# Performance work log

Measured on AMD Instinct MI355X. Metric: run time of the kernel, lower is better.

Reference implementation:

```python
import jax, jax.numpy as jnp
from jax import lax
import numpy as np

B, C, H, W = 16, 3, 512, 512
DICE_W, FOCAL_W, SEP_W = 0.5, 0.5, 0.3
GAMMA, IGNORE, SCALE_IDX, SEP_PW, SMOOTH = 2.0, 255, 2, 1.0, 1e-6


def setup_inputs() -> dict:
    key = jax.random.key(0)
    k1, k2 = jax.random.split(key)
    pred = jax.random.normal(k1, (B, C, H, W), dtype=jnp.float32)
    target = jax.random.randint(k2, (B, H, W), 0, C, dtype=jnp.int32)
    class_weights = jnp.array([0.05, 10.0, 3.0], dtype=jnp.float32)
    return {"pred": pred, "target": target, "class_weights": class_weights}


def _connected_components(mask):
    # mask: [B,H,W] bool -> int32 labels (0 = background), 8-connectivity.
    # Iterative max-label propagation; equivalent component partition to
    # cv2.connectedComponents (label IDs differ but partition is identical,
    # which is all the penalty below depends on).
    m = mask.astype(jnp.int32)
    hw = mask.shape[-2] * mask.shape[-1]
    seeds = jnp.arange(1, hw + 1, dtype=jnp.int32).reshape(1, mask.shape[-2], mask.shape[-1])
    lab0 = m * seeds

    def step(lab):
        nb = lax.reduce_window(lab, jnp.int32(0), lax.max, (1, 3, 3), (1, 1, 1), "SAME")
        return m * nb

    def cond(c):
        lab, prev = c
        return jnp.any(lab != prev)

    def body(c):
        lab, _ = c
        return step(lab), lab

    lab, _ = lax.while_loop(cond, body, (step(lab0), lab0))
    return lab


def _pair_penalty(key_lab, val_lab, both):
    # For each key-label > 0: add 1 if >1 distinct val-labels overlap it.
    # Distinct-count>1 over a set of positive ints  <=>  segment max != segment min.
    n = key_lab.shape[-1] + 1  # labels are raw pixel seeds in [0, H*W]
    BIGI = jnp.int32(2 ** 30)
    vmx_in = jnp.where(both, val_lab, 0)
    vmn_in = jnp.where(both, val_lab, BIGI)

    def per(km, vmx, vmn, b):
        mx = jax.ops.segment_max(vmx, km, num_segments=n)
        mn = jax.ops.segment_min(vmn, km, num_segments=n)
        has = jax.ops.segment_sum(b.astype(jnp.int32), km, num_segments=n) > 0
        hit = has & (mx != mn)
        hit = hit.at[0].set(False)  # exclude background key label 0
        return jnp.sum(hit.astype(jnp.float32))

    return jax.vmap(per)(key_lab, vmx_in, vmn_in, both)


def _separation_loss(pred, target):
    probs = jax.nn.softmax(pred, axis=1)
    pred_bin = probs[:, SCALE_IDX] > 0.5          # [B,H,W]
    tgt_bin = target == SCALE_IDX                 # [B,H,W]
    t_lab = _connected_components(tgt_bin).reshape(pred.shape[0], -1)
    p_lab = _connected_components(pred_bin).reshape(pred.shape[0], -1)
    both = (t_lab > 0) & (p_lab > 0)              # overlap pixels
    pen_t = _pair_penalty(t_lab, p_lab, both)     # target comp split across preds
    pen_p = _pair_penalty(p_lab, t_lab, both)     # pred comp merging targets
    valid = jnp.any(t_lab > 0, axis=1)
    n_valid = jnp.sum(valid.astype(jnp.float32))
    pen = jnp.sum(jnp.where(valid, pen_t + pen_p, 0.0))
    pen = jnp.where(n_valid > 0, pen / jnp.maximum(n_valid * 2.0, 1.0), 0.0)
    nonzero = (jnp.sum(tgt_bin) > 0) & (jnp.sum(pred_bin) > 0)
    return SEP_PW * jnp.where(nonzero, pen, 0.0)


def reference(pred, target, class_weights):
    t = target.astype(jnp.int32)
    tc = jnp.clip(t, 0, C - 1)
    logp = jax.nn.log_softmax(pred, axis=1)                       # [B,C,H,W]
    lp_t = jnp.take_along_axis(logp, tc[:, None], axis=1)[:, 0]    # [B,H,W]
    valid = (t != IGNORE).astype(jnp.float32)
    # weighted cross-entropy with ignore_index (torch semantics: /= sum of weights)
    w = class_weights[tc] * valid
    ce = -jnp.sum(w * lp_t) / jnp.sum(w)
    # dice
    probs = jnp.exp(logp)
    oh = jax.nn.one_hot(t, C, dtype=jnp.float32, axis=1)           # [B,C,H,W]
    inter = jnp.sum(probs * oh, axis=(2, 3))
    union = jnp.sum(probs, axis=(2, 3)) + jnp.sum(oh, axis=(2, 3))
    dice = 1.0 - jnp.mean((2.0 * inter + SMOOTH) / (union + SMOOTH))
    # focal
    pt = jnp.exp(lp_t)
    focal_pix = -class_weights[tc] * (1.0 - pt) ** GAMMA * lp_t * valid
    focal = jnp.sum(focal_pix) / (jnp.sum(valid) + 1e-6)
    # instance separation (non-differentiable; binary threshold + CC)
    sep = _separation_loss(lax.stop_gradient(pred), t)
    return ce + DICE_W * dice + FOCAL_W * focal + SEP_W * sep
```

## Files before the change

kernel.cpp:

```cpp
#include <hip/hip_runtime.h>
#include <stdint.h>


#define NB 16
#define NC 3
#define HH 512
#define WW 512
#define HW (HH * WW)
#define NPIX (NB * HW)
#define LOG2_HW 18
#define IGNORE_IDX 255
#define SCALE_IDX 2
#define SENT (-1)

typedef unsigned long long u64;

struct Accum {
  double ce_num, ce_den, focal_num;
  unsigned long long valid_pix;
  double sum_probs[NB * NC];
  double inter[NB * NC];
  unsigned long long cls_cnt[NB * NC];
  int tcount[NB];
  int pcount[NB];
  int pen[NB];
};

struct Partial {
  double d[9];
  unsigned int u[6];
};

__device__ __forceinline__ double wredd(double v) {
#pragma unroll
  for (int o = 32; o > 0; o >>= 1) v += __shfl_down(v, o, 64);
  return v;
}
__device__ __forceinline__ unsigned int wredu(unsigned int v) {
#pragma unroll
  for (int o = 32; o > 0; o >>= 1) v += __shfl_down(v, o, 64);
  return v;
}

__global__ __launch_bounds__(256) void k_main(
    const float* __restrict__ pred, const int* __restrict__ tgt,
    const float* __restrict__ cw, Partial* __restrict__ part,
    u64* __restrict__ tmask, u64* __restrict__ pmask) {
  const int bid = blockIdx.x;
  const int b = bid >> 6;
  const int chunk = bid & 63;
  const int tid = threadIdx.x;
  const float w0 = cw[0], w1 = cw[1], w2 = cw[2];
  const float* __restrict__ pb = pred + (size_t)b * NC * HW;

  float ce_num = 0.f, ce_den = 0.f, focal = 0.f;
  float sp0 = 0.f, sp1 = 0.f, sp2 = 0.f, it0 = 0.f, it1 = 0.f, it2 = 0.f;
  unsigned int c0 = 0, c1 = 0, c2 = 0, vc = 0, tc_cnt = 0, pc_cnt = 0;

#pragma unroll 1
  for (int k = 0; k < 16; ++k) {
    const int i = (chunk << 12) + (k << 8) + tid;
    const int gp = (b << LOG2_HW) + i;
    const float x0 = pb[i];
    const float x1 = pb[i + HW];
    const float x2 = pb[i + 2 * HW];
    const int t = tgt[gp];

    const float m = fmaxf(fmaxf(x0, x1), x2);
    const float e0 = expf(x0 - m), e1 = expf(x1 - m), e2 = expf(x2 - m);
    const float s = e0 + e1 + e2;
    const float ls = logf(s);
    const float inv = 1.0f / s;
    const float p0 = e0 * inv, p1 = e1 * inv, p2 = e2 * inv;

    sp0 += p0; sp1 += p1; sp2 += p2;

    const int tc = (t < 0) ? 0 : ((t > NC - 1) ? NC - 1 : t);
    const float xt = (tc == 0) ? x0 : ((tc == 1) ? x1 : x2);
    const float lpt = (xt - m) - ls;
    const float pt  = (tc == 0) ? p0 : ((tc == 1) ? p1 : p2);
    const float cwt = (tc == 0) ? w0 : ((tc == 1) ? w1 : w2);
    const float valid = (t != IGNORE_IDX) ? 1.0f : 0.0f;
    const float wv = cwt * valid;

    ce_num += wv * (-lpt);
    ce_den += wv;
    const float om = 1.0f - pt;
    focal += cwt * om * om * (-lpt) * valid;
    vc += (t != IGNORE_IDX) ? 1u : 0u;

    if (t >= 0 && t < NC) {
      if (t == 0)      { it0 += p0; c0++; }
      else if (t == 1) { it1 += p1; c1++; }
      else             { it2 += p2; c2++; }
    }

    const bool tb = (t == SCALE_IDX);
    const float p2soft = e2 / s;
    const bool pbit = (p2soft > 0.5f);
    const u64 mt = __ballot(tb);
    const u64 mp = __ballot(pbit);
    if ((tid & 63) == 0) {
      tmask[gp >> 6] = mt;
      pmask[gp >> 6] = mp;
    }
    tc_cnt += tb ? 1u : 0u;
    pc_cnt += pbit ? 1u : 0u;
  }

  __shared__ double sd[4][9];
  __shared__ unsigned int si[4][6];
  const int wvid = tid >> 6, ln = tid & 63;
  const double r0 = wredd((double)ce_num), r1 = wredd((double)ce_den),
               r2 = wredd((double)focal),
               r3 = wredd((double)sp0), r4 = wredd((double)sp1),
               r5 = wredd((double)sp2),
               r6 = wredd((double)it0), r7 = wredd((double)it1),
               r8 = wredd((double)it2);
  const unsigned int u0 = wredu(c0), u1 = wredu(c1), u2 = wredu(c2),
                     u3 = wredu(vc), u4 = wredu(tc_cnt), u5 = wredu(pc_cnt);
  if (ln == 0) {
    sd[wvid][0] = r0; sd[wvid][1] = r1; sd[wvid][2] = r2;
    sd[wvid][3] = r3; sd[wvid][4] = r4; sd[wvid][5] = r5;
    sd[wvid][6] = r6; sd[wvid][7] = r7; sd[wvid][8] = r8;
    si[wvid][0] = u0; si[wvid][1] = u1; si[wvid][2] = u2;
    si[wvid][3] = u3; si[wvid][4] = u4; si[wvid][5] = u5;
  }
  __syncthreads();
  if (tid == 0) {
    Partial p;
    for (int q = 0; q < 9; ++q) p.d[q] = sd[0][q] + sd[1][q] + sd[2][q] + sd[3][q];
    for (int q = 0; q < 6; ++q) p.u[q] = si[0][q] + si[1][q] + si[2][q] + si[3][q];
    part[bid] = p;
  }
}

__global__ __launch_bounds__(1024) void k_reduce(
    const Partial* __restrict__ part, Accum* __restrict__ acc) {
  const int tid = threadIdx.x;
  const int w = tid >> 6, l = tid & 63;
  const Partial p = part[w * 64 + l];
  double d[9];
  unsigned int u[6];
#pragma unroll
  for (int q = 0; q < 9; ++q) d[q] = wredd(p.d[q]);
#pragma unroll
  for (int q = 0; q < 6; ++q) u[q] = wredu(p.u[q]);

  __shared__ double gsd[16][3];
  __shared__ unsigned int gsu[16];
  if (l == 0) {
    acc->sum_probs[w * NC + 0] = d[3];
    acc->sum_probs[w * NC + 1] = d[4];
    acc->sum_probs[w * NC + 2] = d[5];
    acc->inter[w * NC + 0] = d[6];
    acc->inter[w * NC + 1] = d[7];
    acc->inter[w * NC + 2] = d[8];
    acc->cls_cnt[w * NC + 0] = (unsigned long long)u[0];
    acc->cls_cnt[w * NC + 1] = (unsigned long long)u[1];
    acc->cls_cnt[w * NC + 2] = (unsigned long long)u[2];
    acc->tcount[w] = (int)u[4];
    acc->pcount[w] = (int)u[5];
    gsd[w][0] = d[0]; gsd[w][1] = d[1]; gsd[w][2] = d[2];
    gsu[w] = u[3];
  }
  __syncthreads();
  if (tid == 0) {
    double a0 = 0, a1 = 0, a2 = 0;
    unsigned long long av = 0;
    for (int q = 0; q < 16; ++q) {
      a0 += gsd[q][0]; a1 += gsd[q][1]; a2 += gsd[q][2]; av += gsu[q];
    }
    acc->ce_num = a0; acc->ce_den = a1; acc->focal_num = a2; acc->valid_pix = av;
  }
}

__device__ __forceinline__ int find_lds(volatile int* par, int x) {
  int p = par[x];
  while (p != x) { x = p; p = par[x]; }
  return x;
}
__device__ __forceinline__ void unite_lds(int* par, int a, int b) {
  int la = find_lds(par, a);
  int lb = find_lds(par, b);
  while (la != lb) {
    if (la < lb) { int t = la; la = lb; lb = t; }
    const int old = atomicMin(&par[la], lb);
    if (old == la) break;
    la = old;
  }
}

__global__ __launch_bounds__(256) void k_local(
    const u64* __restrict__ tmask, const u64* __restrict__ pmask,
    int* __restrict__ tlab, int* __restrict__ plab,
    int* __restrict__ tconf, int* __restrict__ pconf) {
  const int idx = blockIdx.x;
  const int img = idx >> 7;
  const int rest = idx & 127;
  const int maskid = rest >> 6;
  const int tile = rest & 63;
  const int ty = tile >> 3, tx = tile & 7;
  const u64* __restrict__ mg = (maskid ? pmask : tmask) + (size_t)img * (HW / 64);
  int* __restrict__ lab  = (maskid ? plab : tlab)   + ((size_t)img << LOG2_HW);
  int* __restrict__ conf = (maskid ? pconf : tconf) + ((size_t)img << LOG2_HW);
  const int tid = threadIdx.x;
  const int lane = tid & 63, wv = tid >> 6;

  __shared__ int par[4096];
  __shared__ u64 mw[64];
  if (tid < 64) mw[tid] = mg[(ty * 64 + tid) * 8 + tx];
  __syncthreads();

#pragma unroll 1
  for (int k = 0; k < 16; ++k) {
    const int y = (k << 2) + wv;
    const u64 w = mw[y];
    int v = -1;
    if ((w >> lane) & 1ull) {
      const u64 sa = w & ~(w << 1);
      const u64 le = sa & (~0ull >> (63 - lane));
      v = (y << 6) + (63 - __clzll(le));
    }
    par[(y << 6) + lane] = v;
  }
  __syncthreads();

#pragma unroll 1
  for (int k = 0; k < 16; ++k) {
    const int y = (k << 2) + wv;
    if (y == 0) continue;
    const u64 w = mw[y];
    if (!((w >> lane) & 1ull)) continue;
    if (lane > 0 && ((w >> (lane - 1)) & 1ull)) continue;
    const u64 z = w >> lane;
    const u64 crun = (z & ~(z + 1)) << lane;
    const u64 win = crun | (crun << 1) | (crun >> 1);
    const u64 a = mw[y - 1];
    u64 aw = a & win;
    const u64 sa = a & ~(a << 1);
    const int me = (y << 6) + lane;
    while (aw) {
      const int p = (int)(__ffsll((long long)aw) - 1);
      const u64 le = sa & (~0ull >> (63 - p));
      const int rs = 63 - __clzll(le);
      unite_lds(par, me, ((y - 1) << 6) + rs);
      const u64 za = a >> p;
      aw &= ~((za & ~(za + 1)) << p);
    }
  }
  __syncthreads();

#pragma unroll 1
  for (int k = 0; k < 16; ++k) {
    const int li = (k << 8) + tid;
    const int y = li >> 6, x = li & 63;
    int out = -1;
    if (par[li] >= 0) {
      int r = par[li], p = par[r];
      while (p != r) { r = p; p = par[r]; }
      out = (ty * 64 + (r >> 6)) * WW + tx * 64 + (r & 63);
    }
    const int gi = (ty * 64 + y) * WW + tx * 64 + x;
    lab[gi] = out;
    conf[gi] = 0;
  }
}

__device__ __forceinline__ int lread(int* p) {
  return __hip_atomic_load(p, __ATOMIC_RELAXED, __HIP_MEMORY_SCOPE_AGENT);
}
__device__ __forceinline__ int findroot(int* L, int x) {
  int p = lread(&L[x]);
  while (p != x) { x = p; p = lread(&L[x]); }
  return x;
}
__device__ __forceinline__ void unite(int* L, int a, int b) {
  int la = findroot(L, a);
  int lb = findroot(L, b);
  while (la != lb) {
    if (la < lb) { int t = la; la = lb; lb = t; }
    const int old = atomicMin(&L[la], lb);
    if (old == la) break;
    la = old;
  }
}

__global__ __launch_bounds__(256) void k_border(int* __restrict__ tlab, int* __restrict__ plab) {
  const int t = blockIdx.x * 256 + threadIdx.x;
  const int pos = t & 511;
  const int rest = t >> 9;
  const int line = rest % 21;
  const int rest2 = rest / 21;
  const int maskid = rest2 & 1;
  const int img = rest2 >> 1;
  int* __restrict__ lab = (maskid ? plab : tlab) + ((size_t)img << LOG2_HW);
  if (line < 7) {
    const int i = (((line + 1) << 6) * WW) + pos;
    if (lab[i] < 0) return;
    if (lab[i - WW] >= 0) unite(lab, i, i - WW);
    if (pos > 0 && lab[i - WW - 1] >= 0) unite(lab, i, i - WW - 1);
    if (pos < WW - 1 && lab[i - WW + 1] >= 0) unite(lab, i, i - WW + 1);
  } else if (line < 14) {
    const int i = pos * WW + ((line - 6) << 6);
    if (lab[i] < 0) return;
    if (lab[i - 1] >= 0) unite(lab, i, i - 1);
    if (pos > 0 && lab[i - WW - 1] >= 0) unite(lab, i, i - WW - 1);
  } else {
    if (pos == 0) return;
    const int i = pos * WW + (((line - 13) << 6) - 1);
    if (lab[i] < 0) return;
    if (lab[i - WW + 1] >= 0) unite(lab, i, i - WW + 1);
  }
}

__device__ __forceinline__ void conf_update(int* __restrict__ conf, int key, int val) {
  const int tag = val + 1;
  const int old = atomicCAS(&conf[key], 0, tag);
  if (old == 0 || old == tag || old == SENT) return;
  atomicExch(&conf[key], SENT);
}

__device__ __forceinline__ int chase_compress(int* __restrict__ L, int i) {
  const int p0 = L[i];
  int r = p0, p = L[r];
  if (p == r) return r;
  do { r = p; p = L[r]; } while (p != r);
  L[p0] = r;
  return r;
}

__global__ __launch_bounds__(256) void k_scatter(
    const u64* __restrict__ tmask, const u64* __restrict__ pmask,
    int* __restrict__ tlab, int* __restrict__ plab,
    int* __restrict__ tconf, int* __restrict__ pconf) {
  const int gt = blockIdx.x * 256 + threadIdx.x;
  const int bb = gt >> LOG2_HW;
  const int i = gt & (HW - 1);
  const size_t base = (size_t)bb << LOG2_HW;
  const int lane = threadIdx.x & 63;
  const u64 tw = tmask[gt >> 6];
  const u64 pw = pmask[gt >> 6];
  if ((tw & pw) == 0) return;
  const bool act = ((tw >> lane) & 1ull) & ((pw >> lane) & 1ull);
  if (!act) return;
  const int rt = chase_compress(tlab + base, i);
  const int rp = chase_compress(plab + base, i);
  conf_update(tconf + base, rt, rp);
  conf_update(pconf + base, rp, rt);
}

__global__ __launch_bounds__(256) void k_count(
    const int4* __restrict__ tconf4, const int4* __restrict__ pconf4,
    int* __restrict__ penpart) {
  const int gt = blockIdx.x * 256 + threadIdx.x;
  const int4 a = tconf4[gt];
  const int4 b = pconf4[gt];
  int add = (a.x == SENT) + (a.y == SENT) + (a.z == SENT) + (a.w == SENT)
          + (b.x == SENT) + (b.y == SENT) + (b.z == SENT) + (b.w == SENT);
  const int tid = threadIdx.x, ln = tid & 63, wv = tid >> 6;
#pragma unroll
  for (int o = 32; o > 0; o >>= 1) add += __shfl_down(add, o, 64);
  __shared__ int s4[4];
  if (ln == 0) s4[wv] = add;
  __syncthreads();
  if (tid == 0) penpart[blockIdx.x] = s4[0] + s4[1] + s4[2] + s4[3];
}

__global__ __launch_bounds__(1024) void k_final(
    const Accum* __restrict__ acc, const int* __restrict__ penpart,
    float* __restrict__ out) {
  const int tid = threadIdx.x, w = tid >> 6, l = tid & 63;
  int s = 0;
#pragma unroll
  for (int k = 0; k < 4; ++k) s += penpart[(w << 8) + (k << 6) + l];
#pragma unroll
  for (int o = 32; o > 0; o >>= 1) s += __shfl_down(s, o, 64);
  __shared__ int pens[16];
  if (l == 0) pens[w] = s;
  __syncthreads();
  if (tid != 0) return;

  const double ce = acc->ce_num / acc->ce_den;
  double dsum = 0.0;
  for (int k = 0; k < NB * NC; ++k) {
    const double un = acc->sum_probs[k] + (double)acc->cls_cnt[k];
    dsum += (2.0 * acc->inter[k] + 1e-6) / (un + 1e-6);
  }
  const double dice = 1.0 - dsum / (double)(NB * NC);
  const double focal = acc->focal_num / ((double)acc->valid_pix + 1e-6);
  long long tt = 0, pp = 0;
  int nv = 0;
  double pensum = 0.0;
  for (int b = 0; b < NB; ++b) {
    tt += acc->tcount[b];
    pp += acc->pcount[b];
    if (acc->tcount[b] > 0) { nv++; pensum += (double)pens[b]; }
  }
  double pen = 0.0;
  if (nv > 0) pen = pensum / fmax((double)nv * 2.0, 1.0);
  const double sep = (tt > 0 && pp > 0) ? 1.0  * pen : 0.0;
  *out = (float)(ce + 0.5 * dice + 0.5 * focal + 0.3 * sep);
}

extern "C" void kernel_launch(void* const* d_in, const int* in_sizes, int n_in,
                              void* d_out, int out_size, void* d_ws, size_t ws_size,
                              hipStream_t stream) {
  (void)in_sizes; (void)n_in; (void)out_size; (void)ws_size;
  const float* pred = (const float*)d_in[0];
  const int* tgt = (const int*)d_in[1];
  const float* cw = (const float*)d_in[2];
  float* out = (float*)d_out;

  char* ws = (char*)d_ws;
  Accum* acc = (Accum*)ws;
  size_t off = 2048;
  Partial* part = (Partial*)(ws + off); off += sizeof(Partial) * NB * 64;
  u64* tmask = (u64*)(ws + off); off += NPIX / 8;
  u64* pmask = (u64*)(ws + off); off += NPIX / 8;
  int* tlab  = (int*)(ws + off); off += (size_t)NPIX * 4;
  int* plab  = (int*)(ws + off); off += (size_t)NPIX * 4;
  int* tconf = (int*)(ws + off); off += (size_t)NPIX * 4;
  int* pconf = (int*)(ws + off); off += (size_t)NPIX * 4;
  int* penpart = (int*)(ws + off); off += (size_t)(NPIX / 1024) * 4;

  hipMemsetAsync(acc, 0, sizeof(Accum), stream);

  k_main<<<NB * 64, 256, 0, stream>>>(pred, tgt, cw, part, tmask, pmask);
  k_reduce<<<1, 1024, 0, stream>>>(part, acc);
  k_local<<<NB * 64 * 2, 256, 0, stream>>>(tmask, pmask, tlab, plab, tconf, pconf);
  k_border<<<(NB * 2 * 21 * 512) / 256, 256, 0, stream>>>(tlab, plab);
  k_scatter<<<NPIX / 256, 256, 0, stream>>>(tmask, pmask, tlab, plab, tconf, pconf);
  k_count<<<NPIX / 1024, 256, 0, stream>>>((const int4*)tconf, (const int4*)pconf, penpart);
  k_final<<<1, 1024, 0, stream>>>(acc, penpart, out);
}
```

Measured before the change: 233.3 us.

## Store tile-local 16-bit labels, sparse root records, fuse count into scatter

Per-pixel labels are now 16-bit tile-local root offsets instead of 32-bit global indices. A parent/conflict int2 record is written only at tile roots, and border unions and scatter lookups work on those root records. Conflict counting moves into the scatter kernel through the atomicExch transition, and the reduce and count kernels plus the memset are removed, with reduction folded into the final kernel. This cuts full-image writes and launches, at the cost of more complex root decoding and uninitialized non-root records that rely on only roots ever being touched.

```diff
diff --git a/kernel.cpp b/kernel.cpp
--- a/kernel.cpp
+++ b/kernel.cpp
@@ -12,19 +12,9 @@
 #define IGNORE_IDX 255
 #define SCALE_IDX 2
 #define SENT (-1)
+#define BG16 0xFFFF
 
 typedef unsigned long long u64;
-
-struct Accum {
-  double ce_num, ce_den, focal_num;
-  unsigned long long valid_pix;
-  double sum_probs[NB * NC];
-  double inter[NB * NC];
-  unsigned long long cls_cnt[NB * NC];
-  int tcount[NB];
-  int pcount[NB];
-  int pen[NB];
-};
 
 struct Partial {
   double d[9];
@@ -135,46 +125,6 @@
   }
 }
 
-__global__ __launch_bounds__(1024) void k_reduce(
-    const Partial* __restrict__ part, Accum* __restrict__ acc) {
-  const int tid = threadIdx.x;
-  const int w = tid >> 6, l = tid & 63;
-  const Partial p = part[w * 64 + l];
-  double d[9];
-  unsigned int u[6];
-#pragma unroll
-  for (int q = 0; q < 9; ++q) d[q] = wredd(p.d[q]);
-#pragma unroll
-  for (int q = 0; q < 6; ++q) u[q] = wredu(p.u[q]);
-
-  __shared__ double gsd[16][3];
-  __shared__ unsigned int gsu[16];
-  if (l == 0) {
-    acc->sum_probs[w * NC + 0] = d[3];
-    acc->sum_probs[w * NC + 1] = d[4];
-    acc->sum_probs[w * NC + 2] = d[5];
-    acc->inter[w * NC + 0] = d[6];
-    acc->inter[w * NC + 1] = d[7];
-    acc->inter[w * NC + 2] = d[8];
-    acc->cls_cnt[w * NC + 0] = (unsigned long long)u[0];
-    acc->cls_cnt[w * NC + 1] = (unsigned long long)u[1];
-    acc->cls_cnt[w * NC + 2] = (unsigned long long)u[2];
-    acc->tcount[w] = (int)u[4];
-    acc->pcount[w] = (int)u[5];
-    gsd[w][0] = d[0]; gsd[w][1] = d[1]; gsd[w][2] = d[2];
-    gsu[w] = u[3];
-  }
-  __syncthreads();
-  if (tid == 0) {
-    double a0 = 0, a1 = 0, a2 = 0;
-    unsigned long long av = 0;
-    for (int q = 0; q < 16; ++q) {
-      a0 += gsd[q][0]; a1 += gsd[q][1]; a2 += gsd[q][2]; av += gsu[q];
-    }
-    acc->ce_num = a0; acc->ce_den = a1; acc->focal_num = a2; acc->valid_pix = av;
-  }
-}
-
 __device__ __forceinline__ int find_lds(volatile int* par, int x) {
   int p = par[x];
   while (p != x) { x = p; p = par[x]; }
@@ -193,8 +143,8 @@
 
 __global__ __launch_bounds__(256) void k_local(
     const u64* __restrict__ tmask, const u64* __restrict__ pmask,
-    int* __restrict__ tlab, int* __restrict__ plab,
-    int* __restrict__ tconf, int* __restrict__ pconf) {
+    ushort* __restrict__ tlab16, ushort* __restrict__ plab16,
+    int2* __restrict__ pc_t, int2* __restrict__ pc_p) {
   const int idx = blockIdx.x;
   const int img = idx >> 7;
   const int rest = idx & 127;
@@ -202,8 +152,8 @@
   const int tile = rest & 63;
   const int ty = tile >> 3, tx = tile & 7;
   const u64* __restrict__ mg = (maskid ? pmask : tmask) + (size_t)img * (HW / 64);
-  int* __restrict__ lab  = (maskid ? plab : tlab)   + ((size_t)img << LOG2_HW);
-  int* __restrict__ conf = (maskid ? pconf : tconf) + ((size_t)img << LOG2_HW);
+  ushort* __restrict__ lab = (maskid ? plab16 : tlab16) + (size_t)img * HW;
+  int2* __restrict__ pc   = (maskid ? pc_p : pc_t) + (size_t)img * HW;
   const int tid = threadIdx.x;
   const int lane = tid & 63, wv = tid >> 6;
 
@@ -252,41 +202,57 @@
   __syncthreads();
 
 #pragma unroll 1
-  for (int k = 0; k < 16; ++k) {
-    const int li = (k << 8) + tid;
-    const int y = li >> 6, x = li & 63;
-    int out = -1;
-    if (par[li] >= 0) {
-      int r = par[li], p = par[r];
-      while (p != r) { r = p; p = par[r]; }
-      out = (ty * 64 + (r >> 6)) * WW + tx * 64 + (r & 63);
-    }
-    const int gi = (ty * 64 + y) * WW + tx * 64 + x;
-    lab[gi] = out;
-    conf[gi] = 0;
-  }
-}
-
-__device__ __forceinline__ int lread(int* p) {
-  return __hip_atomic_load(p, __ATOMIC_RELAXED, __HIP_MEMORY_SCOPE_AGENT);
-}
-__device__ __forceinline__ int findroot(int* L, int x) {
-  int p = lread(&L[x]);
-  while (p != x) { x = p; p = lread(&L[x]); }
+  for (int k = 0; k < 4; ++k) {
+    const int lbase = (k << 10) + (tid << 2);
+    const int gy = (ty << 6) + (lbase >> 6);
+    const int gx = (tx << 6) + (lbase & 63);
+    const int gbase = gy * WW + gx;
+    ushort v[4];
+#pragma unroll
+    for (int j = 0; j < 4; ++j) {
+      const int li = lbase + j;
+      int r = par[li];
+      ushort out = BG16;
+      if (r >= 0) {
+        const bool isroot = (r == li);
+        int p = par[r];
+        while (p != r) { r = p; p = par[r]; }
+        out = (ushort)r;
+        if (isroot) pc[gbase + j] = make_int2(gbase + j, 0);
+      }
+      v[j] = out;
+    }
+    *reinterpret_cast<ushort4*>(&lab[gbase]) =
+        make_ushort4(v[0], v[1], v[2], v[3]);
+  }
+}
+
+__device__ __forceinline__ int pc_par(int2* pc, int x) {
+  return __hip_atomic_load(&pc[x].x, __ATOMIC_RELAXED, __HIP_MEMORY_SCOPE_AGENT);
+}
+__device__ __forceinline__ int findroot_pc(int2* pc, int x) {
+  int p = pc_par(pc, x);
+  while (p != x) { x = p; p = pc_par(pc, x); }
   return x;
 }
-__device__ __forceinline__ void unite(int* L, int a, int b) {
-  int la = findroot(L, a);
-  int lb = findroot(L, b);
+__device__ __forceinline__ void unite_pc(int2* pc, int a, int b) {
+  int la = findroot_pc(pc, a);
+  int lb = findroot_pc(pc, b);
   while (la != lb) {
     if (la < lb) { int t = la; la = lb; lb = t; }
-    const int old = atomicMin(&L[la], lb);
+    const int old = atomicMin(&pc[la].x, lb);
     if (old == la) break;
     la = old;
   }
 }
 
-__global__ __launch_bounds__(256) void k_border(int* __restrict__ tlab, int* __restrict__ plab) {
+__device__ __forceinline__ int decode_root(int ty, int tx, int l) {
+  return ((ty << 6) + (l >> 6)) * WW + (tx << 6) + (l & 63);
+}
+
+__global__ __launch_bounds__(256) void k_border(
+    const ushort* __restrict__ tlab16, const ushort* __restrict__ plab16,
+    int2* __restrict__ pc_t, int2* __restrict__ pc_p) {
   const int t = blockIdx.x * 256 + threadIdx.x;
   const int pos = t & 511;
   const int rest = t >> 9;
@@ -294,108 +260,160 @@
   const int rest2 = rest / 21;
   const int maskid = rest2 & 1;
   const int img = rest2 >> 1;
-  int* __restrict__ lab = (maskid ? plab : tlab) + ((size_t)img << LOG2_HW);
+  const ushort* __restrict__ lab = (maskid ? plab16 : tlab16) + (size_t)img * HW;
+  int2* __restrict__ pc = (maskid ? pc_p : pc_t) + (size_t)img * HW;
+
   if (line < 7) {
-    const int i = (((line + 1) << 6) * WW) + pos;
-    if (lab[i] < 0) return;
-    if (lab[i - WW] >= 0) unite(lab, i, i - WW);
-    if (pos > 0 && lab[i - WW - 1] >= 0) unite(lab, i, i - WW - 1);
-    if (pos < WW - 1 && lab[i - WW + 1] >= 0) unite(lab, i, i - WW + 1);
+    const int y = (line + 1) << 6;
+    const int i = y * WW + pos;
+    const ushort li = lab[i];
+    if (li == BG16) return;
+    const int ty = line + 1, tx = pos >> 6;
+    const int gi = decode_root(ty, tx, li);
+    const ushort ln_ = lab[i - WW];
+    if (ln_ != BG16) unite_pc(pc, gi, decode_root(line, tx, ln_));
+    if (pos > 0) {
+      const ushort lw = lab[i - WW - 1];
+      if (lw != BG16) unite_pc(pc, gi, decode_root(line, (pos - 1) >> 6, lw));
+    }
+    if (pos < WW - 1) {
+      const ushort le = lab[i - WW + 1];
+      if (le != BG16) unite_pc(pc, gi, decode_root(line, (pos + 1) >> 6, le));
+    }
   } else if (line < 14) {
-    const int i = pos * WW + ((line - 6) << 6);
-    if (lab[i] < 0) return;
-    if (lab[i - 1] >= 0) unite(lab, i, i - 1);
-    if (pos > 0 && lab[i - WW - 1] >= 0) unite(lab, i, i - WW - 1);
+    const int x = (line - 6) << 6;
+    const int i = pos * WW + x;
+    const ushort li = lab[i];
+    if (li == BG16) return;
+    const int ty = pos >> 6, tx = line - 6;
+    const int gi = decode_root(ty, tx, li);
+    const ushort lw = lab[i - 1];
+    if (lw != BG16) unite_pc(pc, gi, decode_root(ty, tx - 1, lw));
+    if (pos > 0) {
+      const ushort ld = lab[i - WW - 1];
+      if (ld != BG16) unite_pc(pc, gi, decode_root((pos - 1) >> 6, tx - 1, ld));
+    }
   } else {
     if (pos == 0) return;
-    const int i = pos * WW + (((line - 13) << 6) - 1);
-    if (lab[i] < 0) return;
-    if (lab[i - WW + 1] >= 0) unite(lab, i, i - WW + 1);
-  }
-}
-
-__device__ __forceinline__ void conf_update(int* __restrict__ conf, int key, int val) {
+    const int x = ((line - 13) << 6) - 1;
+    const int i = pos * WW + x;
+    const ushort li = lab[i];
+    if (li == BG16) return;
+    const int ty = pos >> 6, tx = x >> 6;
+    const int gi = decode_root(ty, tx, li);
+    const ushort le = lab[i - WW + 1];
+    if (le != BG16) unite_pc(pc, gi, decode_root((pos - 1) >> 6, tx + 1, le));
+  }
+}
+
+__device__ __forceinline__ int chase_pc(int2* __restrict__ pc, int g) {
+  int r = pc[g].x;
+  if (r == g) return r;
+  int p = pc[r].x;
+  while (p != r) { r = p; p = pc[r].x; }
+  pc[g].x = r;
+  return r;
+}
+
+__device__ __forceinline__ int conf_update(int2* __restrict__ pc, int key, int val) {
   const int tag = val + 1;
-  const int old = atomicCAS(&conf[key], 0, tag);
-  if (old == 0 || old == tag || old == SENT) return;
-  atomicExch(&conf[key], SENT);
-}
-
-__device__ __forceinline__ int chase_compress(int* __restrict__ L, int i) {
-  const int p0 = L[i];
-  int r = p0, p = L[r];
-  if (p == r) return r;
-  do { r = p; p = L[r]; } while (p != r);
-  L[p0] = r;
-  return r;
+  const int old = atomicCAS(&pc[key].y, 0, tag);
+  if (old == 0 || old == tag || old == SENT) return 0;
+  const int prev = atomicExch(&pc[key].y, SENT);
+  return (prev != SENT) ? 1 : 0;
 }
 
 __global__ __launch_bounds__(256) void k_scatter(
-    const u64* __restrict__ tmask, const u64* __restrict__ pmask,
-    int* __restrict__ tlab, int* __restrict__ plab,
-    int* __restrict__ tconf, int* __restrict__ pconf) {
-  const int gt = blockIdx.x * 256 + threadIdx.x;
-  const int bb = gt >> LOG2_HW;
-  const int i = gt & (HW - 1);
-  const size_t base = (size_t)bb << LOG2_HW;
-  const int lane = threadIdx.x & 63;
-  const u64 tw = tmask[gt >> 6];
-  const u64 pw = pmask[gt >> 6];
-  if ((tw & pw) == 0) return;
-  const bool act = ((tw >> lane) & 1ull) & ((pw >> lane) & 1ull);
-  if (!act) return;
-  const int rt = chase_compress(tlab + base, i);
-  const int rp = chase_compress(plab + base, i);
-  conf_update(tconf + base, rt, rp);
-  conf_update(pconf + base, rp, rt);
-}
-
-__global__ __launch_bounds__(256) void k_count(
-    const int4* __restrict__ tconf4, const int4* __restrict__ pconf4,
+    const ushort* __restrict__ tlab16, const ushort* __restrict__ plab16,
+    int2* __restrict__ pc_t, int2* __restrict__ pc_p,
     int* __restrict__ penpart) {
-  const int gt = blockIdx.x * 256 + threadIdx.x;
-  const int4 a = tconf4[gt];
-  const int4 b = pconf4[gt];
-  int add = (a.x == SENT) + (a.y == SENT) + (a.z == SENT) + (a.w == SENT)
-          + (b.x == SENT) + (b.y == SENT) + (b.z == SENT) + (b.w == SENT);
+  const int gt4 = blockIdx.x * 256 + threadIdx.x;
+  const int img = gt4 >> (LOG2_HW - 2);
+  const int i0 = (gt4 & ((HW >> 2) - 1)) << 2;
+  const size_t ibase = (size_t)img * HW;
+  const ushort4 t4 = *reinterpret_cast<const ushort4*>(&tlab16[ibase + i0]);
+  const ushort4 p4 = *reinterpret_cast<const ushort4*>(&plab16[ibase + i0]);
+  int2* __restrict__ pct = pc_t + ibase;
+  int2* __restrict__ pcp = pc_p + ibase;
+  const ushort tl[4] = {t4.x, t4.y, t4.z, t4.w};
+  const ushort pl[4] = {p4.x, p4.y, p4.z, p4.w};
+
+  int cnt = 0;
+  const int y = i0 >> 9, ty = y >> 6, txb = (i0 & 511) >> 6;
+#pragma unroll
+  for (int j = 0; j < 4; ++j) {
+    if (tl[j] != BG16 && pl[j] != BG16) {
+      const int gt_root = decode_root(ty, txb, tl[j]);
+      const int gp_root = decode_root(ty, txb, pl[j]);
+      const int rt = chase_pc(pct, gt_root);
+      const int rp = chase_pc(pcp, gp_root);
+      cnt += conf_update(pct, rt, rp);
+      cnt += conf_update(pcp, rp, rt);
+    }
+  }
+
   const int tid = threadIdx.x, ln = tid & 63, wv = tid >> 6;
 #pragma unroll
-  for (int o = 32; o > 0; o >>= 1) add += __shfl_down(add, o, 64);
+  for (int o = 32; o > 0; o >>= 1) cnt += __shfl_down(cnt, o, 64);
   __shared__ int s4[4];
-  if (ln == 0) s4[wv] = add;
+  if (ln == 0) s4[wv] = cnt;
   __syncthreads();
   if (tid == 0) penpart[blockIdx.x] = s4[0] + s4[1] + s4[2] + s4[3];
 }
 
 __global__ __launch_bounds__(1024) void k_final(
-    const Accum* __restrict__ acc, const int* __restrict__ penpart,
+    const Partial* __restrict__ part, const int* __restrict__ penpart,
     float* __restrict__ out) {
   const int tid = threadIdx.x, w = tid >> 6, l = tid & 63;
+  const Partial p = part[w * 64 + l];
+  double d[9];
+  unsigned int u[6];
+#pragma unroll
+  for (int q = 0; q < 9; ++q) d[q] = wredd(p.d[q]);
+#pragma unroll
+  for (int q = 0; q < 6; ++q) u[q] = wredu(p.u[q]);
+
   int s = 0;
 #pragma unroll
   for (int k = 0; k < 4; ++k) s += penpart[(w << 8) + (k << 6) + l];
 #pragma unroll
   for (int o = 32; o > 0; o >>= 1) s += __shfl_down(s, o, 64);
+
+  __shared__ double imgd[16][9];
+  __shared__ unsigned int imgu[16][6];
   __shared__ int pens[16];
-  if (l == 0) pens[w] = s;
+  if (l == 0) {
+#pragma unroll
+    for (int q = 0; q < 9; ++q) imgd[w][q] = d[q];
+#pragma unroll
+    for (int q = 0; q < 6; ++q) imgu[w][q] = u[q];
+    pens[w] = s;
+  }
   __syncthreads();
   if (tid != 0) return;
 
-  const double ce = acc->ce_num / acc->ce_den;
+  double a0 = 0, a1 = 0, a2 = 0;
+  unsigned long long av = 0;
+  for (int q = 0; q < 16; ++q) {
+    a0 += imgd[q][0]; a1 += imgd[q][1]; a2 += imgd[q][2];
+    av += (unsigned long long)imgu[q][3];
+  }
+  const double ce = a0 / a1;
   double dsum = 0.0;
-  for (int k = 0; k < NB * NC; ++k) {
-    const double un = acc->sum_probs[k] + (double)acc->cls_cnt[k];
-    dsum += (2.0 * acc->inter[k] + 1e-6) / (un + 1e-6);
-  }
+  for (int b = 0; b < NB; ++b)
+    for (int c = 0; c < NC; ++c) {
+      const double un = imgd[b][3 + c] + (double)imgu[b][c];
+      dsum += (2.0 * imgd[b][6 + c] + 1e-6) / (un + 1e-6);
+    }
   const double dice = 1.0 - dsum / (double)(NB * NC);
-  const double focal = acc->focal_num / ((double)acc->valid_pix + 1e-6);
+  const double focal = a2 / ((double)av + 1e-6);
   long long tt = 0, pp = 0;
   int nv = 0;
   double pensum = 0.0;
   for (int b = 0; b < NB; ++b) {
-    tt += acc->tcount[b];
-    pp += acc->pcount[b];
-    if (acc->tcount[b] > 0) { nv++; pensum += (double)pens[b]; }
+    tt += imgu[b][4];
+    pp += imgu[b][5];
+    if (imgu[b][4] > 0) { nv++; pensum += (double)pens[b]; }
   }
   double pen = 0.0;
   if (nv > 0) pen = pensum / fmax((double)nv * 2.0, 1.0);
@@ -413,24 +431,19 @@
   float* out = (float*)d_out;
 
   char* ws = (char*)d_ws;
-  Accum* acc = (Accum*)ws;
-  size_t off = 2048;
+  size_t off = 0;
   Partial* part = (Partial*)(ws + off); off += sizeof(Partial) * NB * 64;
   u64* tmask = (u64*)(ws + off); off += NPIX / 8;
   u64* pmask = (u64*)(ws + off); off += NPIX / 8;
-  int* tlab  = (int*)(ws + off); off += (size_t)NPIX * 4;
-  int* plab  = (int*)(ws + off); off += (size_t)NPIX * 4;
-  int* tconf = (int*)(ws + off); off += (size_t)NPIX * 4;
-  int* pconf = (int*)(ws + off); off += (size_t)NPIX * 4;
+  ushort* tlab16 = (ushort*)(ws + off); off += (size_t)NPIX * 2;
+  ushort* plab16 = (ushort*)(ws + off); off += (size_t)NPIX * 2;
+  int2* pc_t = (int2*)(ws + off); off += (size_t)NPIX * 8;
+  int2* pc_p = (int2*)(ws + off); off += (size_t)NPIX * 8;
   int* penpart = (int*)(ws + off); off += (size_t)(NPIX / 1024) * 4;
 
-  hipMemsetAsync(acc, 0, sizeof(Accum), stream);
-
   k_main<<<NB * 64, 256, 0, stream>>>(pred, tgt, cw, part, tmask, pmask);
-  k_reduce<<<1, 1024, 0, stream>>>(part, acc);
-  k_local<<<NB * 64 * 2, 256, 0, stream>>>(tmask, pmask, tlab, plab, tconf, pconf);
-  k_border<<<(NB * 2 * 21 * 512) / 256, 256, 0, stream>>>(tlab, plab);
-  k_scatter<<<NPIX / 256, 256, 0, stream>>>(tmask, pmask, tlab, plab, tconf, pconf);
-  k_count<<<NPIX / 1024, 256, 0, stream>>>((const int4*)tconf, (const int4*)pconf, penpart);
-  k_final<<<1, 1024, 0, stream>>>(acc, penpart, out);
-}
+  k_local<<<NB * 64 * 2, 256, 0, stream>>>(tmask, pmask, tlab16, plab16, pc_t, pc_p);
+  k_border<<<(NB * 2 * 21 * 512) / 256, 256, 0, stream>>>(tlab16, plab16, pc_t, pc_p);
+  k_scatter<<<NPIX / 1024, 256, 0, stream>>>(tlab16, plab16, pc_t, pc_p, penpart);
+  k_final<<<1, 1024, 0, stream>>>(part, penpart, out);
+}
```

Result: slower. 243.9 us (+4.5%).
